# Performance work log

Measured on AMD Instinct MI355X. Metric: run time of the kernel, lower is better.

Reference implementation:

```python
import jax, jax.numpy as jnp
import numpy as np

B, S, D, H = 2, 2048, 768, 12
DH = D // H  # 64


def setup_inputs() -> dict:
    key = jax.random.key(0)
    ks = jax.random.split(key, 6)
    sd = 1.0 / np.sqrt(D)
    x = jax.random.normal(ks[0], (B, S, 3 * D), dtype=jnp.float32)
    # causal additive mask: 1.0 where attention is disallowed (future positions)
    mask = jnp.triu(jnp.ones((S, S), dtype=jnp.float32), k=1)[None, None, :, :]
    return {
        "x": x,
        "mask": mask,
        "wq": jax.random.normal(ks[1], (D, D), dtype=jnp.float32) * sd,
        "bq": jnp.zeros((D,), dtype=jnp.float32),
        "wk": jax.random.normal(ks[2], (D, D), dtype=jnp.float32) * sd,
        "bk": jnp.zeros((D,), dtype=jnp.float32),
        "wv": jax.random.normal(ks[3], (D, D), dtype=jnp.float32) * sd,
        "bv": jnp.zeros((D,), dtype=jnp.float32),
        "wc": jax.random.normal(ks[4], (D, D), dtype=jnp.float32) * sd,
        "bc": jnp.zeros((D,), dtype=jnp.float32),
    }


def _split_heads(t):
    # [B, S, D] -> [B, H, S, DH]
    return t.reshape(B, S, H, DH).transpose(0, 2, 1, 3)


def reference(x, mask, wq, bq, wk, bk, wv, bv, wc, bc):
    xq, xk, xv = jnp.split(x, 3, axis=-1)
    q = _split_heads(xq @ wq + bq)
    k = _split_heads(xk @ wk + bk)
    v = _split_heads(xv @ wv + bv)
    scores = jnp.einsum("bhqd,bhkd->bhqk", q, k) / jnp.sqrt(jnp.float32(DH))
    scores = scores + mask * (-1e9)
    attn = jax.nn.softmax(scores, axis=-1)
    out = jnp.einsum("bhqk,bhkd->bhqd", attn, v)
    out = out.transpose(0, 2, 1, 3).reshape(B, S, D)  # merge heads
    return out @ wc + bc
```

## Files before the change

### kernel.cpp

```cpp
#include <hip/hip_runtime.h>
#include <math.h>

#define S_LEN   2048
#define D_MODEL 768
#define NH      12
#define DH      64
#define BATCH   2

typedef __attribute__((ext_vector_type(4)))  float f32x4;
typedef __attribute__((ext_vector_type(16))) float f32x16;
typedef __attribute__((ext_vector_type(8)))  short bf16x8;
typedef __attribute__((ext_vector_type(4)))  short short4v;
typedef __attribute__((ext_vector_type(2)))  unsigned u32x2;

__device__ __forceinline__ short f2bf(float f) {
    union { float f; unsigned u; } v; v.f = f;
    unsigned r = (v.u + 0x7FFFu + ((v.u >> 16) & 1u)) >> 16;
    return (short)r;
}
__device__ __forceinline__ float bf2f(short s) {
    union { unsigned u; float f; } v; v.u = ((unsigned)(unsigned short)s) << 16;
    return v.f;
}
__device__ __forceinline__ unsigned cvt_pk_bf16(float lo, float hi) {
    unsigned r;
    asm("v_cvt_pk_bf16_f32 %0, %1, %2" : "=v"(r) : "v"(lo), "v"(hi));
    return r;
}
__device__ __forceinline__ void perm32swap(unsigned &a, unsigned &b) {
    asm("v_permlane32_swap_b32 %0, %1" : "+v"(a), "+v"(b));
}

#define GLOAD_LDS16(gp, lp)                                                     \
    __builtin_amdgcn_global_load_lds(                                           \
        (const __attribute__((address_space(1))) void*)(gp),                    \
        (__attribute__((address_space(3))) void*)(lp), 16, 0, 0)

__global__ __launch_bounds__(256) void convert_xw_kernel(
    const float* __restrict__ x, short* __restrict__ xb,
    const float* __restrict__ wq, const float* __restrict__ wk,
    const float* __restrict__ wv, const float* __restrict__ wc,
    short* __restrict__ wt)
{
    const int bid = blockIdx.x;
    const int t = threadIdx.x;
    if (bid < 4608) {
        const size_t i = ((size_t)bid * 256 + t) * 8;
        const f32x4 a = *(const f32x4*)(x + i);
        const f32x4 b = *(const f32x4*)(x + i + 4);
        bf16x8 r;
        r[0] = f2bf(a[0]); r[1] = f2bf(a[1]); r[2] = f2bf(a[2]); r[3] = f2bf(a[3]);
        r[4] = f2bf(b[0]); r[5] = f2bf(b[1]); r[6] = f2bf(b[2]); r[7] = f2bf(b[3]);
        *(bf16x8*)(xb + i) = r;
        return;
    }
    __shared__ float Ld[64][65];
    const int rem = bid - 4608;
    const int z  = rem / 144;
    const int yy = (rem % 144) / 12;
    const int xx = rem % 12;
    const float* W = (z == 0) ? wq : (z == 1) ? wk : (z == 2) ? wv : wc;
    short* dst = wt + (size_t)z * D_MODEL * D_MODEL;
    const int r0 = yy * 64;
    const int c0 = xx * 64;

#pragma unroll
    for (int i = 0; i < 4; ++i) {
        const int r = (t >> 4) + 16 * i;
        const int c = (t & 15) * 4;
        const float4 a = *(const float4*)(W + (size_t)(r0 + r) * D_MODEL + c0 + c);
        Ld[r][c + 0] = a.x; Ld[r][c + 1] = a.y; Ld[r][c + 2] = a.z; Ld[r][c + 3] = a.w;
    }
    __syncthreads();
#pragma unroll
    for (int i = 0; i < 4; ++i) {
        const int n = (t >> 4) + 16 * i;
        const int kq = (t & 15) * 4;
        short4v s4;
        s4[0] = f2bf(Ld[kq + 0][n]); s4[1] = f2bf(Ld[kq + 1][n]);
        s4[2] = f2bf(Ld[kq + 2][n]); s4[3] = f2bf(Ld[kq + 3][n]);
        *(short4v*)(dst + (size_t)(c0 + n) * D_MODEL + r0 + kq) = s4;
    }
}

__device__ __forceinline__ void gemm_bt_body(
    const short* __restrict__ A, int lda,
    const short* __restrict__ Bt,
    const float* __restrict__ bias,
    void* __restrict__ C, int ldc, int out_mode)
{
    __shared__ __align__(16) char ldsA[16384];
    __shared__ __align__(16) char ldsB[16384];

    const int t = threadIdx.x, lane = t & 63, w = t >> 6;
    const int l15 = lane & 15, l4 = lane >> 4;
    const int wr = w >> 1, wc = w & 1;
    const int row0 = blockIdx.y * 128, col0 = blockIdx.x * 128;

    const int srow = lane >> 3;
    const int sblk = (lane & 7) ^ srow;

    f32x4 acc[4][4];
#pragma unroll
    for (int i = 0; i < 4; ++i)
#pragma unroll
        for (int j = 0; j < 4; ++j) acc[i][j] = (f32x4){0.f, 0.f, 0.f, 0.f};

    for (int kt = 0; kt < 12; ++kt) {
        __syncthreads();
#pragma unroll
        for (int i = 0; i < 4; ++i) {
            const int row = i * 32 + w * 8 + srow;
            GLOAD_LDS16(A  + (size_t)(row0 + row) * lda + kt * 64 + sblk * 8,
                        ldsA + i * 4096 + w * 1024);
            GLOAD_LDS16(Bt + (size_t)(col0 + row) * D_MODEL + kt * 64 + sblk * 8,
                        ldsB + i * 4096 + w * 1024);
        }
        __syncthreads();

        bf16x8 af[4][2], bfr[4][2];
#pragma unroll
        for (int rb = 0; rb < 4; ++rb) {
            const int r = wr * 64 + rb * 16 + l15;
#pragma unroll
            for (int c = 0; c < 2; ++c)
                af[rb][c] = *(const bf16x8*)(ldsA + r * 128 + (((c * 4 + l4) ^ (r & 7)) << 4));
        }
#pragma unroll
        for (int cb = 0; cb < 4; ++cb) {
            const int r = wc * 64 + cb * 16 + l15;
#pragma unroll
            for (int c = 0; c < 2; ++c)
                bfr[cb][c] = *(const bf16x8*)(ldsB + r * 128 + (((c * 4 + l4) ^ (r & 7)) << 4));
        }
        __builtin_amdgcn_s_setprio(1);
#pragma unroll
        for (int rb = 0; rb < 4; ++rb)
#pragma unroll
            for (int cb = 0; cb < 4; ++cb) {
                acc[rb][cb] = __builtin_amdgcn_mfma_f32_16x16x32_bf16(
                    af[rb][0], bfr[cb][0], acc[rb][cb], 0, 0, 0);
                acc[rb][cb] = __builtin_amdgcn_mfma_f32_16x16x32_bf16(
                    af[rb][1], bfr[cb][1], acc[rb][cb], 0, 0, 0);
            }
        __builtin_amdgcn_s_setprio(0);
    }

#pragma unroll
    for (int cb = 0; cb < 4; ++cb) {
        const int col = col0 + wc * 64 + cb * 16 + l15;
        const float bv = bias[col];
        if (out_mode == 2) {
            const int h  = col >> 6, dh = col & 63;
#pragma unroll
            for (int rb = 0; rb < 4; ++rb) {
                const int row = row0 + wr * 64 + rb * 16 + 4 * l4;
                const int b   = row >> 11, s0 = row & 2047;
                short4v s4;
                s4[0] = f2bf(acc[rb][cb][0] + bv);
                s4[1] = f2bf(acc[rb][cb][1] + bv);
                s4[2] = f2bf(acc[rb][cb][2] + bv);
                s4[3] = f2bf(acc[rb][cb][3] + bv);
                *(short4v*)((short*)C + ((size_t)((b * 12 + h) * 64 + dh)) * S_LEN + s0) = s4;
            }
        } else {
#pragma unroll
            for (int rb = 0; rb < 4; ++rb)
#pragma unroll
                for (int r = 0; r < 4; ++r) {
                    const int row = row0 + wr * 64 + rb * 16 + 4 * l4 + r;
                    const float val = acc[rb][cb][r] + bv;
                    if (out_mode == 1) ((short*)C)[(size_t)row * ldc + col] = f2bf(val);
                    else               ((float*)C)[(size_t)row * ldc + col] = val;
                }
        }
    }
}

__global__ __launch_bounds__(256) void qkv_gemm_kernel(
    const short* __restrict__ xb, const short* __restrict__ wt,
    const float* __restrict__ bq, const float* __restrict__ bk,
    const float* __restrict__ bv, short* __restrict__ qkv)
{
    const int which = blockIdx.z;
    const float* bias = (which == 0) ? bq : (which == 1) ? bk : bv;
    gemm_bt_body(xb + which * D_MODEL, 3 * D_MODEL,
                 wt + (size_t)which * D_MODEL * D_MODEL, bias,
                 qkv + (size_t)which * BATCH * S_LEN * D_MODEL, D_MODEL,
                 (which == 2) ? 2 : 1);
}

__global__ __launch_bounds__(256) void proj_gemm_kernel(
    const short* __restrict__ att, const short* __restrict__ wct,
    const float* __restrict__ bc, float* __restrict__ out)
{
    gemm_bt_body(att, D_MODEL, wct, bc, out, D_MODEL, 0);
}

__global__ __launch_bounds__(512, 4) void attn_mfma_kernel(
    const short* __restrict__ q, const short* __restrict__ k,
    const short* __restrict__ vt, short* __restrict__ o)
{
    __shared__ __align__(16) char bufK[2][2][8192];
    __shared__ __align__(16) char bufV[2][2][8192];
    __shared__ float mlx[2][128];

    const int t    = threadIdx.x;
    const int lane = t & 63;
    const int w    = t >> 6;
    const int g    = w >> 2;
    const int w4   = w & 3;
    const int l31  = lane & 31;
    const int hi   = lane >> 5;
    const int r7   = l31 & 7;

    const int h  = blockIdx.y;
    const int b  = blockIdx.z;
    const int bh = h + 12 * b;
    const int qt = (bh >= 16) ? (15 - (int)blockIdx.x) : (int)blockIdx.x;
    const int nt = qt + 1;

    const size_t base   = (size_t)b * (S_LEN * D_MODEL) + h * DH;
    const size_t vtbase = (size_t)bh * DH * S_LEN;
    const int q0 = qt * 128 + w4 * 32;

    bf16x8 qf[4];
    {
        const short* qp = q + base + (size_t)(q0 + l31) * D_MODEL + 8 * hi;
#pragma unroll
        for (int dc = 0; dc < 4; ++dc) {
            bf16x8 r = *(const bf16x8*)(qp + 16 * dc);
#pragma unroll
            for (int j = 0; j < 8; ++j) r[j] = f2bf(bf2f(r[j]) * 0.125f);
            qf[dc] = r;
        }
    }

    f32x16 oT[2];
    oT[0] = (f32x16)(0.f); oT[1] = (f32x16)(0.f);
    float mrun = -1e30f, lrun = 0.f;

    const int srow = lane >> 3;
    const int sblk = (lane & 7) ^ srow;

    {
        const int tk0 = g * nt;
#pragma unroll
        for (int i = 0; i < 2; ++i) {
            const int row = i * 32 + w4 * 8 + srow;
            GLOAD_LDS16(k  + base   + (size_t)(tk0 * 64 + row) * D_MODEL + sblk * 8,
                        bufK[g][0] + i * 4096 + w4 * 1024);
            GLOAD_LDS16(vt + vtbase + (size_t)row * S_LEN + tk0 * 64 + sblk * 8,
                        bufV[g][0] + i * 4096 + w4 * 1024);
        }
        __syncthreads();
    }

    for (int i = 0; i < nt; ++i) {
        const int cur = i & 1, nxt = cur ^ 1;
        const bool have_next = (i + 1 < nt);
        const int tk = g * nt + i;

        if (have_next) {
            const int tkn = tk + 1;
#pragma unroll
            for (int j = 0; j < 2; ++j) {
                const int row = j * 32 + w4 * 8 + srow;
                GLOAD_LDS16(k  + base   + (size_t)(tkn * 64 + row) * D_MODEL + sblk * 8,
                            bufK[g][nxt] + (size_t)(j * 4096 + w4 * 1024));
                GLOAD_LDS16(vt + vtbase + (size_t)row * S_LEN + tkn * 64 + sblk * 8,
                            bufV[g][nxt] + (size_t)(j * 4096 + w4 * 1024));
            }
        }

        if (tk * 64 <= q0 + 31) {
            f32x16 cS[2];
            __builtin_amdgcn_s_setprio(1);
#pragma unroll
            for (int s = 0; s < 2; ++s) {
                f32x16 acc = (f32x16)(0.f);
#pragma unroll
                for (int dc = 0; dc < 4; ++dc) {
                    const int row = 32 * s + l31;
                    const bf16x8 kf = *(const bf16x8*)(
                        bufK[g][cur] + row * 128 + (((unsigned)(32 * dc + 16 * hi)) ^ ((unsigned)r7 << 4)));
                    acc = __builtin_amdgcn_mfma_f32_32x32x16_bf16(kf, qf[dc], acc, 0, 0, 0);
                }
                cS[s] = acc;
            }
            __builtin_amdgcn_s_setprio(0);

            if (tk * 64 + 63 > q0) {
                const int qg = q0 + l31;
#pragma unroll
                for (int s = 0; s < 2; ++s)
#pragma unroll
                    for (int rg = 0; rg < 16; ++rg) {
                        const int key = tk * 64 + 32 * s + (rg & 3) + 8 * (rg >> 2) + 4 * hi;
                        if (key > qg) cS[s][rg] = -1e30f;
                    }
            }

            float pmax = -1e30f;
#pragma unroll
            for (int s = 0; s < 2; ++s)
#pragma unroll
                for (int rg = 0; rg < 16; ++rg) pmax = fmaxf(pmax, cS[s][rg]);
            pmax = fmaxf(pmax, __shfl_xor(pmax, 32));

            if (!__all(pmax - mrun <= 8.0f)) {
                const float mnew = fmaxf(mrun, pmax);
                const float corr = __expf(mrun - mnew);
                lrun *= corr;
#pragma unroll
                for (int d0 = 0; d0 < 2; ++d0)
#pragma unroll
                    for (int rg = 0; rg < 16; ++rg) oT[d0][rg] *= corr;
                mrun = mnew;
            }
            float psum = 0.f;
#pragma unroll
            for (int s = 0; s < 2; ++s)
#pragma unroll
                for (int rg = 0; rg < 16; ++rg) {
                    const float e = __expf(cS[s][rg] - mrun);
                    cS[s][rg] = e; psum += e;
                }
            psum += __shfl_xor(psum, 32);
            lrun += psum;

            bf16x8 pfrag[4];
#pragma unroll
            for (int s = 0; s < 2; ++s)
#pragma unroll
                for (int tt = 0; tt < 2; ++tt) {
                    unsigned a0 = cvt_pk_bf16(cS[s][8 * tt + 0], cS[s][8 * tt + 1]);
                    unsigned a1 = cvt_pk_bf16(cS[s][8 * tt + 2], cS[s][8 * tt + 3]);
                    unsigned b0 = cvt_pk_bf16(cS[s][8 * tt + 4], cS[s][8 * tt + 5]);
                    unsigned b1 = cvt_pk_bf16(cS[s][8 * tt + 6], cS[s][8 * tt + 7]);
                    perm32swap(a0, b0);
                    perm32swap(a1, b1);
                    union { unsigned u[4]; bf16x8 v8; } pk;
                    pk.u[0] = a0; pk.u[1] = a1; pk.u[2] = b0; pk.u[3] = b1;
                    pfrag[2 * s + tt] = pk.v8;
                }

            __builtin_amdgcn_s_setprio(1);
#pragma unroll
            for (int d0 = 0; d0 < 2; ++d0) {
                f32x16 acc = oT[d0];
#pragma unroll
                for (int c = 0; c < 4; ++c) {
                    const int row = 32 * d0 + l31;
                    const bf16x8 vf = *(const bf16x8*)(
                        bufV[g][cur] + row * 128 + (((unsigned)(32 * c + 16 * hi)) ^ ((unsigned)r7 << 4)));
                    acc = __builtin_amdgcn_mfma_f32_32x32x16_bf16(vf, pfrag[c], acc, 0, 0, 0);
                }
                oT[d0] = acc;
            }
            __builtin_amdgcn_s_setprio(0);
        }
        __syncthreads();
    }

    if (g == 1) {
        float* ex = (float*)(&bufK[0][0][0]) + w4 * 2048;
#pragma unroll
        for (int d0 = 0; d0 < 2; ++d0)
#pragma unroll
            for (int rg = 0; rg < 16; ++rg)
                ex[(d0 * 16 + rg) * 64 + lane] = oT[d0][rg];
        if (hi == 0) {
            mlx[0][w4 * 32 + l31] = mrun;
            mlx[1][w4 * 32 + l31] = lrun;
        }
    }
    __syncthreads();

    if (g == 0) {
        const float m1  = mlx[0][w4 * 32 + l31];
        const float l1v = mlx[1][w4 * 32 + l31];
        const float M   = fmaxf(mrun, m1);
        const float a0  = __expf(mrun - M);
        const float a1  = __expf(m1 - M);
        const float inv = 1.f / (a0 * lrun + a1 * l1v);
        const float* ex = (const float*)(&bufK[0][0][0]) + w4 * 2048;

        char* wbuf = (char*)(&bufV[0][0][0]) + w4 * 4096;
#pragma unroll
        for (int d0 = 0; d0 < 2; ++d0)
#pragma unroll
            for (int gg = 0; gg < 4; ++gg) {
                float c0v = (a0 * oT[d0][4 * gg + 0] + a1 * ex[(d0 * 16 + 4 * gg + 0) * 64 + lane]) * inv;
                float c1v = (a0 * oT[d0][4 * gg + 1] + a1 * ex[(d0 * 16 + 4 * gg + 1) * 64 + lane]) * inv;
                float c2v = (a0 * oT[d0][4 * gg + 2] + a1 * ex[(d0 * 16 + 4 * gg + 2) * 64 + lane]) * inv;
                float c3v = (a0 * oT[d0][4 * gg + 3] + a1 * ex[(d0 * 16 + 4 * gg + 3) * 64 + lane]) * inv;
                u32x2 u2;
                u2[0] = cvt_pk_bf16(c0v, c1v);
                u2[1] = cvt_pk_bf16(c2v, c3v);
                const unsigned byteoff = ((unsigned)(16 * gg + 8 * hi + 64 * d0)) ^ ((unsigned)r7 << 4);
                *(u32x2*)(wbuf + l31 * 128 + byteoff) = u2;
            }
#pragma unroll
        for (int it = 0; it < 4; ++it) {
            const int R = lane >> 1;
            const unsigned lb = ((unsigned)((lane & 1) * 16 + it * 32)) ^ ((unsigned)(R & 7) << 4);
            const bf16x8 vv = *(const bf16x8*)(wbuf + R * 128 + lb);
            const int row = qt * 128 + w4 * 32 + R;
            const int col = (lane & 1) * 8 + it * 16;
            *(bf16x8*)(o + base + (size_t)row * D_MODEL + col) = vv;
        }
    }
}

extern "C" void kernel_launch(void* const* d_in, const int* in_sizes, int n_in,
                              void* d_out, int out_size, void* d_ws, size_t ws_size,
                              hipStream_t stream)
{
    const float* x  = (const float*)d_in[0];
    const float* wq = (const float*)d_in[2];
    const float* bq = (const float*)d_in[3];
    const float* wk = (const float*)d_in[4];
    const float* bk = (const float*)d_in[5];
    const float* wv = (const float*)d_in[6];
    const float* bv = (const float*)d_in[7];
    const float* wc = (const float*)d_in[8];
    const float* bc = (const float*)d_in[9];
    float* out = (float*)d_out;

    const size_t nx  = (size_t)BATCH * S_LEN * 3 * D_MODEL;
    const size_t nw  = (size_t)D_MODEL * D_MODEL;
    const size_t nqv = (size_t)BATCH * S_LEN * D_MODEL;

    short* xb  = (short*)d_ws;
    short* wt  = xb + nx;
    short* qkv = wt + 4 * nw;
    short* att = qkv + 3 * nqv;

    dim3 blk(256);
    convert_xw_kernel<<<dim3(4608 + 576), blk, 0, stream>>>(x, xb, wq, wk, wv, wc, wt);
    qkv_gemm_kernel  <<<dim3(6, 32, 3), blk, 0, stream>>>(xb, wt, bq, bk, bv, qkv);
    attn_mfma_kernel <<<dim3(16, NH, BATCH), dim3(512), 0, stream>>>(
        qkv, qkv + nqv, qkv + 2 * nqv, att);
    proj_gemm_kernel <<<dim3(6, 32), blk, 0, stream>>>(att, wt + 3 * nw, bc, out);
}
```

Baseline: 103.5 us.

## Split attention key range across four wave groups and use exp2 softmax

Doubles the attention block to 1024 threads so four groups of waves each process a quarter of the causal key tiles, instead of two groups each taking half. The partial results are merged through LDS with a four-way log-sum-exp combine. Exponentials switch to the hardware exp2 instruction, with log2(e) folded into the Q pre-scale and the rescale threshold adjusted to match. Output is now written straight from registers as 8-byte stores rather than staged through LDS. The cost is 128KB of shared memory per block, which limits occupancy, plus a more expensive merge step and less-coalesced global stores.

```diff
diff --git a/kernel.cpp b/kernel.cpp
--- a/kernel.cpp
+++ b/kernel.cpp
@@ -11,7 +11,6 @@
 typedef __attribute__((ext_vector_type(16))) float f32x16;
 typedef __attribute__((ext_vector_type(8)))  short bf16x8;
 typedef __attribute__((ext_vector_type(4)))  short short4v;
-typedef __attribute__((ext_vector_type(2)))  unsigned u32x2;
 
 __device__ __forceinline__ short f2bf(float f) {
     union { float f; unsigned u; } v; v.f = f;
@@ -29,6 +28,11 @@
 }
 __device__ __forceinline__ void perm32swap(unsigned &a, unsigned &b) {
     asm("v_permlane32_swap_b32 %0, %1" : "+v"(a), "+v"(b));
+}
+__device__ __forceinline__ float exp2_fast(float x) {
+    float r;
+    asm("v_exp_f32 %0, %1" : "=v"(r) : "v"(x));
+    return r;
 }
 
 #define GLOAD_LDS16(gp, lp)                                                     \
@@ -197,13 +201,12 @@
     gemm_bt_body(att, D_MODEL, wct, bc, out, D_MODEL, 0);
 }
 
-__global__ __launch_bounds__(512, 4) void attn_mfma_kernel(
+__global__ __launch_bounds__(1024, 4) void attn_mfma_kernel(
     const short* __restrict__ q, const short* __restrict__ k,
     const short* __restrict__ vt, short* __restrict__ o)
 {
-    __shared__ __align__(16) char bufK[2][2][8192];
-    __shared__ __align__(16) char bufV[2][2][8192];
-    __shared__ float mlx[2][128];
+    __shared__ __align__(16) char smem[131072];
+    __shared__ float mlx[4][2][128];
 
     const int t    = threadIdx.x;
     const int lane = t & 63;
@@ -218,20 +221,26 @@
     const int b  = blockIdx.z;
     const int bh = h + 12 * b;
     const int qt = (bh >= 16) ? (15 - (int)blockIdx.x) : (int)blockIdx.x;
-    const int nt = qt + 1;
+    const int nkt = 2 * qt + 2;
+    const int cpg = (2 * qt + 5) >> 2;
+    const int t0g = g * cpg;
 
     const size_t base   = (size_t)b * (S_LEN * D_MODEL) + h * DH;
     const size_t vtbase = (size_t)bh * DH * S_LEN;
     const int q0 = qt * 128 + w4 * 32;
 
+    char* myK = smem + g * 32768;
+    char* myV = smem + g * 32768 + 16384;
+
     bf16x8 qf[4];
     {
+        const float qscale = 0.18033688f;
         const short* qp = q + base + (size_t)(q0 + l31) * D_MODEL + 8 * hi;
 #pragma unroll
         for (int dc = 0; dc < 4; ++dc) {
             bf16x8 r = *(const bf16x8*)(qp + 16 * dc);
 #pragma unroll
-            for (int j = 0; j < 8; ++j) r[j] = f2bf(bf2f(r[j]) * 0.125f);
+            for (int j = 0; j < 8; ++j) r[j] = f2bf(bf2f(r[j]) * qscale);
             qf[dc] = r;
         }
     }
@@ -243,37 +252,38 @@
     const int srow = lane >> 3;
     const int sblk = (lane & 7) ^ srow;
 
-    {
-        const int tk0 = g * nt;
+    if (t0g < nkt) {
 #pragma unroll
         for (int i = 0; i < 2; ++i) {
             const int row = i * 32 + w4 * 8 + srow;
-            GLOAD_LDS16(k  + base   + (size_t)(tk0 * 64 + row) * D_MODEL + sblk * 8,
-                        bufK[g][0] + i * 4096 + w4 * 1024);
-            GLOAD_LDS16(vt + vtbase + (size_t)row * S_LEN + tk0 * 64 + sblk * 8,
-                        bufV[g][0] + i * 4096 + w4 * 1024);
-        }
-        __syncthreads();
-    }
-
-    for (int i = 0; i < nt; ++i) {
+            GLOAD_LDS16(k  + base   + (size_t)(t0g * 64 + row) * D_MODEL + sblk * 8,
+                        myK + i * 4096 + w4 * 1024);
+            GLOAD_LDS16(vt + vtbase + (size_t)row * S_LEN + t0g * 64 + sblk * 8,
+                        myV + i * 4096 + w4 * 1024);
+        }
+    }
+    __syncthreads();
+
+    for (int i = 0; i < cpg; ++i) {
         const int cur = i & 1, nxt = cur ^ 1;
-        const bool have_next = (i + 1 < nt);
-        const int tk = g * nt + i;
-
-        if (have_next) {
+        const int tk = t0g + i;
+
+        if (i + 1 < cpg && tk + 1 < nkt) {
             const int tkn = tk + 1;
 #pragma unroll
             for (int j = 0; j < 2; ++j) {
                 const int row = j * 32 + w4 * 8 + srow;
                 GLOAD_LDS16(k  + base   + (size_t)(tkn * 64 + row) * D_MODEL + sblk * 8,
-                            bufK[g][nxt] + (size_t)(j * 4096 + w4 * 1024));
+                            myK + nxt * 8192 + j * 4096 + w4 * 1024);
                 GLOAD_LDS16(vt + vtbase + (size_t)row * S_LEN + tkn * 64 + sblk * 8,
-                            bufV[g][nxt] + (size_t)(j * 4096 + w4 * 1024));
-            }
-        }
-
-        if (tk * 64 <= q0 + 31) {
+                            myV + nxt * 8192 + j * 4096 + w4 * 1024);
+            }
+        }
+
+        if (tk < nkt && tk * 64 <= q0 + 31) {
+            const char* bk_ = myK + cur * 8192;
+            const char* bv_ = myV + cur * 8192;
+
             f32x16 cS[2];
             __builtin_amdgcn_s_setprio(1);
 #pragma unroll
@@ -283,7 +293,7 @@
                 for (int dc = 0; dc < 4; ++dc) {
                     const int row = 32 * s + l31;
                     const bf16x8 kf = *(const bf16x8*)(
-                        bufK[g][cur] + row * 128 + (((unsigned)(32 * dc + 16 * hi)) ^ ((unsigned)r7 << 4)));
+                        bk_ + row * 128 + (((unsigned)(32 * dc + 16 * hi)) ^ ((unsigned)r7 << 4)));
                     acc = __builtin_amdgcn_mfma_f32_32x32x16_bf16(kf, qf[dc], acc, 0, 0, 0);
                 }
                 cS[s] = acc;
@@ -308,9 +318,9 @@
                 for (int rg = 0; rg < 16; ++rg) pmax = fmaxf(pmax, cS[s][rg]);
             pmax = fmaxf(pmax, __shfl_xor(pmax, 32));
 
-            if (!__all(pmax - mrun <= 8.0f)) {
+            if (!__all(pmax - mrun <= 11.52f)) {
                 const float mnew = fmaxf(mrun, pmax);
-                const float corr = __expf(mrun - mnew);
+                const float corr = exp2_fast(mrun - mnew);
                 lrun *= corr;
 #pragma unroll
                 for (int d0 = 0; d0 < 2; ++d0)
@@ -323,7 +333,7 @@
             for (int s = 0; s < 2; ++s)
 #pragma unroll
                 for (int rg = 0; rg < 16; ++rg) {
-                    const float e = __expf(cS[s][rg] - mrun);
+                    const float e = exp2_fast(cS[s][rg] - mrun);
                     cS[s][rg] = e; psum += e;
                 }
             psum += __shfl_xor(psum, 32);
@@ -353,7 +363,7 @@
                 for (int c = 0; c < 4; ++c) {
                     const int row = 32 * d0 + l31;
                     const bf16x8 vf = *(const bf16x8*)(
-                        bufV[g][cur] + row * 128 + (((unsigned)(32 * c + 16 * hi)) ^ ((unsigned)r7 << 4)));
+                        bv_ + row * 128 + (((unsigned)(32 * c + 16 * hi)) ^ ((unsigned)r7 << 4)));
                     acc = __builtin_amdgcn_mfma_f32_32x32x16_bf16(vf, pfrag[c], acc, 0, 0, 0);
                 }
                 oT[d0] = acc;
@@ -363,53 +373,57 @@
         __syncthreads();
     }
 
-    if (g == 1) {
-        float* ex = (float*)(&bufK[0][0][0]) + w4 * 2048;
+    if (g >= 1) {
+        const float pscale = (lrun > 0.f) ? (1.f / lrun) : 0.f;
+        float* ex = (float*)smem + (size_t)((g - 1) * 4 + w4) * 2048;
 #pragma unroll
         for (int d0 = 0; d0 < 2; ++d0)
 #pragma unroll
             for (int rg = 0; rg < 16; ++rg)
-                ex[(d0 * 16 + rg) * 64 + lane] = oT[d0][rg];
+                ex[(d0 * 16 + rg) * 64 + lane] = oT[d0][rg] * pscale;
         if (hi == 0) {
-            mlx[0][w4 * 32 + l31] = mrun;
-            mlx[1][w4 * 32 + l31] = lrun;
+            mlx[g][0][w4 * 32 + l31] = mrun;
+            mlx[g][1][w4 * 32 + l31] = lrun;
         }
     }
     __syncthreads();
 
     if (g == 0) {
-        const float m1  = mlx[0][w4 * 32 + l31];
-        const float l1v = mlx[1][w4 * 32 + l31];
-        const float M   = fmaxf(mrun, m1);
-        const float a0  = __expf(mrun - M);
-        const float a1  = __expf(m1 - M);
-        const float inv = 1.f / (a0 * lrun + a1 * l1v);
-        const float* ex = (const float*)(&bufK[0][0][0]) + w4 * 2048;
-
-        char* wbuf = (char*)(&bufV[0][0][0]) + w4 * 4096;
+        const int row = w4 * 32 + l31;
+        const float m1 = mlx[1][0][row], l1 = mlx[1][1][row];
+        const float m2 = mlx[2][0][row], l2 = mlx[2][1][row];
+        const float m3 = mlx[3][0][row], l3 = mlx[3][1][row];
+        float M = fmaxf(fmaxf(mrun, m1), fmaxf(m2, m3));
+        const float w0 = exp2_fast(mrun - M) * lrun;
+        const float w1 = exp2_fast(m1 - M) * l1;
+        const float w2 = exp2_fast(m2 - M) * l2;
+        const float w3 = exp2_fast(m3 - M) * l3;
+        const float inv = 1.f / (w0 + w1 + w2 + w3);
+        const float c0 = exp2_fast(mrun - M) * inv;
+        const float c1 = w1 * inv, c2 = w2 * inv, c3 = w3 * inv;
+
+        const float* ex1 = (const float*)smem + (size_t)(0 * 4 + w4) * 2048;
+        const float* ex2 = (const float*)smem + (size_t)(1 * 4 + w4) * 2048;
+        const float* ex3 = (const float*)smem + (size_t)(2 * 4 + w4) * 2048;
+
+        const int qrow = qt * 128 + row;
+        short* orow = o + base + (size_t)qrow * D_MODEL;
 #pragma unroll
         for (int d0 = 0; d0 < 2; ++d0)
 #pragma unroll
             for (int gg = 0; gg < 4; ++gg) {
-                float c0v = (a0 * oT[d0][4 * gg + 0] + a1 * ex[(d0 * 16 + 4 * gg + 0) * 64 + lane]) * inv;
-                float c1v = (a0 * oT[d0][4 * gg + 1] + a1 * ex[(d0 * 16 + 4 * gg + 1) * 64 + lane]) * inv;
-                float c2v = (a0 * oT[d0][4 * gg + 2] + a1 * ex[(d0 * 16 + 4 * gg + 2) * 64 + lane]) * inv;
-                float c3v = (a0 * oT[d0][4 * gg + 3] + a1 * ex[(d0 * 16 + 4 * gg + 3) * 64 + lane]) * inv;
-                u32x2 u2;
-                u2[0] = cvt_pk_bf16(c0v, c1v);
-                u2[1] = cvt_pk_bf16(c2v, c3v);
-                const unsigned byteoff = ((unsigned)(16 * gg + 8 * hi + 64 * d0)) ^ ((unsigned)r7 << 4);
-                *(u32x2*)(wbuf + l31 * 128 + byteoff) = u2;
-            }
-#pragma unroll
-        for (int it = 0; it < 4; ++it) {
-            const int R = lane >> 1;
-            const unsigned lb = ((unsigned)((lane & 1) * 16 + it * 32)) ^ ((unsigned)(R & 7) << 4);
-            const bf16x8 vv = *(const bf16x8*)(wbuf + R * 128 + lb);
-            const int row = qt * 128 + w4 * 32 + R;
-            const int col = (lane & 1) * 8 + it * 16;
-            *(bf16x8*)(o + base + (size_t)row * D_MODEL + col) = vv;
-        }
+                short4v s4;
+#pragma unroll
+                for (int j = 0; j < 4; ++j) {
+                    const int rg = 4 * gg + j;
+                    const int ix = (d0 * 16 + rg) * 64 + lane;
+                    const float val = c0 * oT[d0][rg]
+                                    + c1 * ex1[ix] + c2 * ex2[ix] + c3 * ex3[ix];
+                    s4[j] = f2bf(val);
+                }
+                const int dh0 = 32 * d0 + 8 * gg + 4 * hi;
+                *(short4v*)(orow + dh0) = s4;
+            }
     }
 }
 
@@ -440,7 +454,7 @@
     dim3 blk(256);
     convert_xw_kernel<<<dim3(4608 + 576), blk, 0, stream>>>(x, xb, wq, wk, wv, wc, wt);
     qkv_gemm_kernel  <<<dim3(6, 32, 3), blk, 0, stream>>>(xb, wt, bq, bk, bv, qkv);
-    attn_mfma_kernel <<<dim3(16, NH, BATCH), dim3(512), 0, stream>>>(
+    attn_mfma_kernel <<<dim3(16, NH, BATCH), dim3(1024), 0, stream>>>(
         qkv, qkv + nqv, qkv + 2 * nqv, att);
     proj_gemm_kernel <<<dim3(6, 32), blk, 0, stream>>>(att, wt + 3 * nw, bc, out);
 }
```

After: 111.1 us. 1.07x slower.
